# Performance work log

Hardware: AMD Instinct MI355X
Metric: run time of the kernel (lower is better)

## Reference

```python
import jax, jax.numpy as jnp
import numpy as np

B, N, DIM = 4, 2048, 768
H, C = 12, 64            # num_heads, head_dim
M = 384                  # num random features = dim * kernel_ratio
SCALE = C ** (-0.25)
EPS = 1e-8
INV_SQRT_M = 1.0 / np.sqrt(M).astype(np.float32)


def _make_orf(key):
    # per-head orthogonal random features: rows of each (C, M) block are
    # orthonormal (C <= M), scaled by sqrt(M), matching sample_orf's intent.
    g = jax.random.normal(key, (H, M, C), jnp.float32)
    q = jnp.linalg.qr(g)[0]                 # (H, M, C), orthonormal columns
    return jnp.transpose(q, (0, 2, 1)) * np.float32(np.sqrt(M))  # (H, C, M)


def setup_inputs() -> dict:
    key = jax.random.key(0)
    k0, k1, k2, k3 = jax.random.split(key, 4)
    x = jax.random.normal(k0, (B, N, DIM), jnp.float32)
    w = _make_orf(k1)                                       # (H, C, M), frozen
    Wqkv = jax.random.normal(k2, (DIM, 3 * DIM), jnp.float32) * 0.02
    Wproj = jax.random.normal(k3, (DIM, DIM), jnp.float32) * 0.02
    bproj = jnp.zeros((DIM,), jnp.float32)
    return {"x": x, "w": w, "Wqkv": Wqkv, "Wproj": Wproj, "bproj": bproj}


def _kernel(x, w):
    # x: (B, H, N, C) -> phi(x): (B, H, N, M)
    xs = x * SCALE
    proj = jnp.einsum('bhnc,hcm->bhnm', xs, w)
    sq_half = 0.5 * jnp.sum(xs * xs, axis=-1, keepdims=True)  # (B,H,N,1)
    return jnp.exp(proj - sq_half) * INV_SQRT_M


def reference(x, w, Wqkv, Wproj, bproj):
    qkv = (x @ Wqkv).reshape(B, N, 3, H, C).transpose(2, 0, 3, 1, 4)
    q, k, v = qkv[0], qkv[1], qkv[2]
    qf = _kernel(q, w)                       # (B, H, N, M)
    kf = _kernel(k, w)                       # (B, H, N, M)
    # normalizer D_n = q'_n . sum_j k'_j
    D = jnp.einsum('bhnm,bhm->bhn', qf, jnp.sum(kf, axis=2)) + EPS
    # linear attention: (k'^T v) then q' @ (k'^T v)
    ktv = jnp.einsum('bhnm,bhnc->bhmc', kf, v)      # (B, H, M, C)
    out = jnp.einsum('bhnm,bhmc->bhnc', qf, ktv) / D[..., None]
    out = out.transpose(0, 2, 1, 3).reshape(B, N, DIM)
    return out @ Wproj + bproj
```

## Files before the change

kernel.cpp:

```cpp
#include <hip/hip_runtime.h>

typedef __attribute__((ext_vector_type(8))) short s16x8;
typedef __attribute__((ext_vector_type(4))) float f32x4;

#define MFMA(a, b, c) __builtin_amdgcn_mfma_f32_16x16x32_bf16(a, b, c, 0, 0, 0)

namespace {

constexpr int Bn = 4, Nn = 2048, Hn = 12, Mn = 384;
constexpr float SCALE = 0.35355339059327379f;
constexpr float EPS = 1e-8f;
constexpr float SC2 = 0.51012051755958393f;
constexpr float SQC2 = 0.090169742829486635f;

__device__ inline unsigned short f2b(float f) {
  unsigned u = __builtin_bit_cast(unsigned, f);
  return (unsigned short)((u + 0x7fffu + ((u >> 16) & 1u)) >> 16);
}
__device__ inline float b2f(unsigned short h) {
  unsigned u = ((unsigned)h) << 16;
  return __builtin_bit_cast(float, u);
}

__device__ inline void gl_lds16(const unsigned short* g, unsigned short* l) {
  __builtin_amdgcn_global_load_lds(
      (const __attribute__((address_space(1))) unsigned int*)g,
      (__attribute__((address_space(3))) unsigned int*)l, 16, 0, 0);
}

__device__ inline void tr_cvt_64(const float* __restrict__ src, int sld,
                                 unsigned short* __restrict__ dst, int dld,
                                 float* lds ) {
  const int t = threadIdx.x;
  const int r = t >> 4, cq = (t & 15) * 4;
#pragma unroll
  for (int p = 0; p < 4; ++p) {
    const int k = p * 16 + r;
    const float4 v = *(const float4*)(src + (size_t)k * sld + cq);
    lds[k * 65 + cq + 0] = v.x;
    lds[k * 65 + cq + 1] = v.y;
    lds[k * 65 + cq + 2] = v.z;
    lds[k * 65 + cq + 3] = v.w;
  }
  __syncthreads();
  const int n = t >> 2, kq = (t & 3) * 16;
  s16x8 o0, o1;
#pragma unroll
  for (int j = 0; j < 8; ++j) {
    o0[j] = (short)f2b(lds[(kq + j) * 65 + n]);
    o1[j] = (short)f2b(lds[(kq + 8 + j) * 65 + n]);
  }
  *(s16x8*)(dst + (size_t)n * dld + kq) = o0;
  *(s16x8*)(dst + (size_t)n * dld + kq + 8) = o1;
}

__global__ __launch_bounds__(256) void cvt_all_k(const float* __restrict__ x,
                                                 const float* __restrict__ Wqkv,
                                                 const float* __restrict__ Wproj,
                                                 const float* __restrict__ w,
                                                 unsigned short* __restrict__ xb,
                                                 unsigned short* __restrict__ wqT,
                                                 unsigned short* __restrict__ wpT,
                                                 unsigned short* __restrict__ wt) {
  __shared__ float lds[64 * 65];
  const int bid = blockIdx.x;
  if (bid < 3072) {
    const int id = bid * 256 + threadIdx.x;
    const float* src = x + (size_t)id * 8;
    s16x8 o;
#pragma unroll
    for (int j = 0; j < 8; ++j) o[j] = (short)f2b(src[j]);
    *(s16x8*)(xb + (size_t)id * 8) = o;
  } else if (bid < 3504) {
    const int tid = bid - 3072;
    const int k0 = (tid % 12) * 64, n0 = (tid / 12) * 64;
    tr_cvt_64(Wqkv + (size_t)k0 * 2304 + n0, 2304, wqT + (size_t)n0 * 768 + k0, 768, lds);
  } else if (bid < 3648) {
    const int tid = bid - 3504;
    const int k0 = (tid % 12) * 64, n0 = (tid / 12) * 64;
    tr_cvt_64(Wproj + (size_t)k0 * 768 + n0, 768, wpT + (size_t)n0 * 768 + k0, 768, lds);
  } else {
    const int tid = bid - 3648;
    const int h = tid / 6, m0 = (tid % 6) * 64;
    tr_cvt_64(w + (size_t)h * 64 * 384 + m0, 384, wt + ((size_t)h * 384 + m0) * 64, 64, lds);
  }
}

__global__ __launch_bounds__(256) void gemm_qkv_k(const unsigned short* __restrict__ A,
                                                  const unsigned short* __restrict__ Bt,
                                                  unsigned short* __restrict__ obf) {
  __shared__ unsigned short ldsA[128 * 64];
  __shared__ unsigned short ldsB[128 * 64];
  char* lA = (char*)ldsA;
  char* lB = (char*)ldsB;
  const int t = threadIdx.x, lane = t & 63, w = t >> 6;
  const int ln = lane & 15, kg = lane >> 4;
  const int flat = blockIdx.y * 18 + blockIdx.x;
  const int swz = (flat & 7) * 144 + (flat >> 3);
  const size_t bm = (size_t)(swz / 18) * 128, bn = (size_t)(swz % 18) * 128;
  const int wr = w >> 1, wc = w & 1;
  const int sr = lane >> 3, s = lane & 7;
  f32x4 acc[4][4];
#pragma unroll
  for (int i = 0; i < 4; ++i)
#pragma unroll
    for (int j = 0; j < 4; ++j) acc[i][j] = (f32x4){0.f, 0.f, 0.f, 0.f};

  for (int kb = 0; kb < 768; kb += 64) {
    __syncthreads();
#pragma unroll
    for (int c = 0; c < 4; ++c) {
      const int row = c * 32 + w * 8 + sr;
      const int ss = (s ^ (row & 7)) * 8;
      gl_lds16(A + (bm + row) * 768 + kb + ss, ldsA + (c * 4 + w) * 512);
      gl_lds16(Bt + (bn + row) * 768 + kb + ss, ldsB + (c * 4 + w) * 512);
    }
    __syncthreads();
#pragma unroll
    for (int ks = 0; ks < 2; ++ks) {
      s16x8 af[4], bfr[4];
#pragma unroll
      for (int mi = 0; mi < 4; ++mi) {
        const int row = wr * 64 + mi * 16 + ln;
        af[mi] = *(const s16x8*)(lA + row * 128 + (((ks * 4 + kg) ^ (row & 7)) << 4));
      }
#pragma unroll
      for (int ni = 0; ni < 4; ++ni) {
        const int row = wc * 64 + ni * 16 + ln;
        bfr[ni] = *(const s16x8*)(lB + row * 128 + (((ks * 4 + kg) ^ (row & 7)) << 4));
      }
#pragma unroll
      for (int mi = 0; mi < 4; ++mi)
#pragma unroll
        for (int ni = 0; ni < 4; ++ni) acc[mi][ni] = MFMA(af[mi], bfr[ni], acc[mi][ni]);
    }
  }
#pragma unroll
  for (int mi = 0; mi < 4; ++mi)
#pragma unroll
    for (int ni = 0; ni < 4; ++ni) {
      const size_t orow0 = bm + wr * 64 + mi * 16 + kg * 4;
      const size_t ocol = bn + wc * 64 + ni * 16 + ln;
#pragma unroll
      for (int r = 0; r < 4; ++r) obf[(orow0 + r) * 2304 + ocol] = f2b(acc[mi][ni][r]);
    }
}

__global__ __launch_bounds__(256) void gemm_proj_k(const unsigned short* __restrict__ A,
                                                   const unsigned short* __restrict__ Bt,
                                                   float* __restrict__ out,
                                                   const float* __restrict__ bias) {
  __shared__ unsigned short ldsA[128 * 64];
  __shared__ unsigned short ldsB[64 * 64];
  char* lA = (char*)ldsA;
  char* lB = (char*)ldsB;
  const int t = threadIdx.x, lane = t & 63, w = t >> 6;
  const int ln = lane & 15, kg = lane >> 4;
  const int flat = blockIdx.y * 12 + blockIdx.x;
  const int swz = (flat & 7) * 96 + (flat >> 3);
  const size_t bm = (size_t)(swz / 12) * 128, bn = (size_t)(swz % 12) * 64;
  const int wr = w >> 1, wc = w & 1;
  const int sr = lane >> 3, s = lane & 7;
  f32x4 acc[4][2];
#pragma unroll
  for (int i = 0; i < 4; ++i)
#pragma unroll
    for (int j = 0; j < 2; ++j) acc[i][j] = (f32x4){0.f, 0.f, 0.f, 0.f};

  for (int kb = 0; kb < 768; kb += 64) {
    __syncthreads();
#pragma unroll
    for (int c = 0; c < 4; ++c) {
      const int row = c * 32 + w * 8 + sr;
      const int ss = (s ^ (row & 7)) * 8;
      gl_lds16(A + (bm + row) * 768 + kb + ss, ldsA + (c * 4 + w) * 512);
    }
#pragma unroll
    for (int c = 0; c < 2; ++c) {
      const int row = c * 32 + w * 8 + sr;
      const int ss = (s ^ (row & 7)) * 8;
      gl_lds16(Bt + (bn + row) * 768 + kb + ss, ldsB + (c * 4 + w) * 512);
    }
    __syncthreads();
#pragma unroll
    for (int ks = 0; ks < 2; ++ks) {
      s16x8 af[4], bfr[2];
#pragma unroll
      for (int mi = 0; mi < 4; ++mi) {
        const int row = wr * 64 + mi * 16 + ln;
        af[mi] = *(const s16x8*)(lA + row * 128 + (((ks * 4 + kg) ^ (row & 7)) << 4));
      }
#pragma unroll
      for (int ni = 0; ni < 2; ++ni) {
        const int row = wc * 32 + ni * 16 + ln;
        bfr[ni] = *(const s16x8*)(lB + row * 128 + (((ks * 4 + kg) ^ (row & 7)) << 4));
      }
#pragma unroll
      for (int mi = 0; mi < 4; ++mi)
#pragma unroll
        for (int ni = 0; ni < 2; ++ni) acc[mi][ni] = MFMA(af[mi], bfr[ni], acc[mi][ni]);
    }
  }
#pragma unroll
  for (int mi = 0; mi < 4; ++mi)
#pragma unroll
    for (int ni = 0; ni < 2; ++ni) {
      const size_t orow0 = bm + wr * 64 + mi * 16 + kg * 4;
      const size_t ocol = bn + wc * 32 + ni * 16 + ln;
      const float bv = bias[ocol];
#pragma unroll
      for (int r = 0; r < 4; ++r) out[(orow0 + r) * 768 + ocol] = acc[mi][ni][r] + bv;
    }
}

template <int NCT, int CT0>
__device__ inline void s2_gemm2(const char* kfT_b, const char* vt_b, int mts, int ln, int kg,
                                f32x4 (*acc)[3]) {
#pragma unroll
  for (int half = 0; half < 2; ++half) {
    s16x8 a[3], bb[NCT];
#pragma unroll
    for (int j = 0; j < 3; ++j) {
      const int m = (mts + j) * 16 + ln;
      a[j] = *(const s16x8*)(kfT_b + m * 128 + ((half * 64 + kg * 16) ^ ((m & 7) << 4)));
    }
#pragma unroll
    for (int i = 0; i < NCT; ++i) {
      const int c = (CT0 + i) * 16 + ln;
      bb[i] = *(const s16x8*)(vt_b + c * 128 + ((half * 64 + kg * 16) ^ ((c & 7) << 4)));
    }
#pragma unroll
    for (int j = 0; j < 3; ++j)
#pragma unroll
      for (int i = 0; i < NCT; ++i) acc[j][i] = MFMA(a[j], bb[i], acc[j][i]);
  }
}

__global__ __launch_bounds__(512, 4) void stage2_k(const unsigned short* __restrict__ qkv,
                                                   const unsigned short* __restrict__ wt,
                                                   float* __restrict__ ktv_part,
                                                   float* __restrict__ ksum_part) {
  __shared__ unsigned short kfT[192 * 64];
  __shared__ unsigned short vt[2][80 * 64];
  __shared__ unsigned short wt_s[192 * 64];
  __shared__ unsigned short k_s[64 * 64];
  char* kfT_b = (char*)kfT;
  char* wt_b = (char*)wt_s;
  char* k_b = (char*)k_s;
  const int t = threadIdx.x, lane = t & 63, w = t >> 6;
  const int ln = lane & 15, kg = lane >> 4;
  const int gx = blockIdx.x, h = blockIdx.y, b = blockIdx.z;
  const int ng = gx >> 1, mh = gx & 1, m0 = mh * 192;
  const int bh = b * Hn + h;
  const int ntile = w & 3, mgrp = w >> 2;
  const int mts = (w & 3) * 3;
  const int cg = w >> 2;
  const int lr = lane >> 3, sl = lane & 7;

  auto stage_k = [&](int ch) {
    const int row = w * 8 + lr;
    gl_lds16(qkv + ((size_t)b * Nn + ng * 256 + ch * 64 + row) * 2304 + 768 + h * 64 +
                 ((sl ^ (row & 7)) * 8),
             k_s + w * 512);
  };
  const int vn = t >> 3, vc0 = (t & 7) * 8;
  auto load_v = [&](int ch) {
    return *(const s16x8*)(qkv + ((size_t)b * Nn + ng * 256 + ch * 64 + vn) * 2304 + 1536 +
                           h * 64 + vc0);
  };
  auto scat_v = [&](s16x8 vv, int buf) {
    char* vb = (char*)vt[buf];
#pragma unroll
    for (int j = 0; j < 8; ++j) {
      const int c = vc0 + j;
      *(unsigned short*)(vb + c * 128 + ((2 * vn) ^ ((c & 7) << 4))) = (unsigned short)vv[j];
    }
  };

#pragma unroll
  for (int rr = 0; rr < 3; ++rr) {
    const int j = w * 3 + rr;
    const int row = j * 8 + lr;
    gl_lds16(wt + ((size_t)h * 384 + m0 + row) * 64 + ((sl ^ (row & 7)) * 8), wt_s + j * 512);
  }
  for (int i = t; i < 2048; i += 512) {
    const int buf = i >> 10, r = i & 1023;
    const int c = 64 + (r >> 6), nn = r & 63;
    *(unsigned short*)((char*)vt[buf] + c * 128 + ((2 * nn) ^ ((c & 7) << 4))) =
        (c == 64) ? (unsigned short)0x3F80 : (unsigned short)0;
  }
  stage_k(0);
  s16x8 vreg = load_v(0);
  __syncthreads();
  scat_v(vreg, 0);
  __syncthreads();

  f32x4 acc[3][3];
#pragma unroll
  for (int j = 0; j < 3; ++j)
#pragma unroll
    for (int i = 0; i < 3; ++i) acc[j][i] = (f32x4){0.f, 0.f, 0.f, 0.f};

  for (int ch = 0; ch < 4; ++ch) {
    {
      const int arow = ntile * 16 + ln;
      const s16x8 a0 = *(const s16x8*)(k_b + arow * 128 + ((kg ^ (arow & 7)) << 4));
      const s16x8 a1 = *(const s16x8*)(k_b + arow * 128 + (((kg + 4) ^ (arow & 7)) << 4));
      float sq = 0.f;
#pragma unroll
      for (int j = 0; j < 8; ++j) {
        const float f0 = b2f((unsigned short)a0[j]);
        const float f1 = b2f((unsigned short)a1[j]);
        sq = fmaf(f0, f0, sq);
        sq = fmaf(f1, f1, sq);
      }
      sq += __shfl_xor(sq, 16);
      sq += __shfl_xor(sq, 32);
      const int kg4 = (lane >> 4) << 2;
      float sqv[4];
#pragma unroll
      for (int r = 0; r < 4; ++r) sqv[r] = SQC2 * __shfl(sq, kg4 + r);
#pragma unroll
      for (int i = 0; i < 6; ++i) {
        const int mloc = (mgrp * 6 + i) * 16 + ln;
        const s16x8 b0 = *(const s16x8*)(wt_b + mloc * 128 + ((kg ^ (mloc & 7)) << 4));
        const s16x8 b1 = *(const s16x8*)(wt_b + mloc * 128 + (((kg + 4) ^ (mloc & 7)) << 4));
        f32x4 p = (f32x4){0.f, 0.f, 0.f, 0.f};
        p = MFMA(a0, b0, p);
        p = MFMA(a1, b1, p);
        const float e0 = exp2f(fmaf(SC2, p[0], -sqv[0]));
        const float e1 = exp2f(fmaf(SC2, p[1], -sqv[1]));
        const float e2 = exp2f(fmaf(SC2, p[2], -sqv[2]));
        const float e3 = exp2f(fmaf(SC2, p[3], -sqv[3]));
        uint2 pk;
        pk.x = (unsigned)f2b(e0) | ((unsigned)f2b(e1) << 16);
        pk.y = (unsigned)f2b(e2) | ((unsigned)f2b(e3) << 16);
        const int bytn = 32 * ntile + 8 * kg;
        *(uint2*)(kfT_b + mloc * 128 + (bytn ^ ((mloc & 7) << 4))) = pk;
      }
    }
    __syncthreads();
    if (ch < 3) {
      stage_k(ch + 1);
      vreg = load_v(ch + 1);
    }
    const char* vt_cur = (const char*)vt[ch & 1];
    if (cg == 0)
      s2_gemm2<3, 0>(kfT_b, vt_cur, mts, ln, kg, acc);
    else
      s2_gemm2<2, 3>(kfT_b, vt_cur, mts, ln, kg, acc);
    if (ch < 3) scat_v(vreg, (ch + 1) & 1);
    __syncthreads();
  }
  float* base = ktv_part + ((size_t)ng * 48 + bh) * (384 * 64);
  const int nct2 = cg ? 2 : 3, ct0c = cg ? 3 : 0;
#pragma unroll
  for (int j = 0; j < 3; ++j)
#pragma unroll
    for (int i = 0; i < 3; ++i) {
      if (i >= nct2) continue;
      const int ct = ct0c + i;
      const int mrow0 = m0 + (mts + j) * 16 + kg * 4;
      if (ct < 4) {
        const int c = ct * 16 + ln;
#pragma unroll
        for (int r = 0; r < 4; ++r) base[(size_t)(mrow0 + r) * 64 + c] = acc[j][i][r];
      } else if (ln == 0) {
#pragma unroll
        for (int r = 0; r < 4; ++r)
          ksum_part[((size_t)ng * 48 + bh) * 384 + mrow0 + r] = acc[j][i][r];
      }
    }
}

__global__ __launch_bounds__(256) void reduce_all_k(const float* __restrict__ part,
                                                    const float* __restrict__ partk,
                                                    unsigned short* __restrict__ ktve) {
  __shared__ float lds[64 * 65];
  const int bid = blockIdx.x;
  const int t = threadIdx.x;
  if (bid < 288) {
    const int bh = bid / 6, m0 = (bid % 6) * 64;
    const size_t gs = (size_t)48 * 24576;
    const int c = t & 63, mr = t >> 6;
#pragma unroll
    for (int p = 0; p < 16; ++p) {
      const int m = p * 4 + mr;
      const size_t o = ((size_t)bh * 384 + m0 + m) * 64 + c;
      float s = 0.f;
#pragma unroll
      for (int g = 0; g < 8; ++g) s += part[o + (size_t)g * gs];
      lds[c * 65 + m] = s;
    }
    __syncthreads();
    const int cr = t >> 2, mq = (t & 3) * 16;
    s16x8 o0, o1;
#pragma unroll
    for (int j = 0; j < 8; ++j) {
      o0[j] = (short)f2b(lds[cr * 65 + mq + j]);
      o1[j] = (short)f2b(lds[cr * 65 + mq + 8 + j]);
    }
    unsigned short* dst = ktve + ((size_t)bh * 80 + cr) * 384 + m0 + mq;
    *(s16x8*)dst = o0;
    *(s16x8*)(dst + 8) = o1;
  } else {
    const int idx = (bid - 288) * 256 + t;
    const int bh = idx / 384, m = idx % 384;
    const int gk = 48 * 384;
    float s = 0.f;
#pragma unroll
    for (int g = 0; g < 8; ++g) s += partk[idx + g * gk];
    const unsigned short hi = f2b(s);
    const unsigned short lo = f2b(s - b2f(hi));
    const size_t base = ((size_t)bh * 80 + 64) * 384 + m;
    ktve[base] = hi;
    ktve[base + 384] = lo;
  }
}

__global__ __launch_bounds__(512, 4) void stage3_k(const unsigned short* __restrict__ qkv,
                                                   const unsigned short* __restrict__ wt,
                                                   const unsigned short* __restrict__ ktve,
                                                   unsigned short* __restrict__ attn) {
  __shared__ unsigned short q_s[128 * 64];
  __shared__ unsigned short qf_s[128 * 64];
  __shared__ unsigned short wt_s[2][64 * 64];
  __shared__ unsigned short kt_s[2][80 * 64];
  char* q_b = (char*)q_s;
  char* qf_b = (char*)qf_s;
  const int t = threadIdx.x, lane = t & 63, w = t >> 6;
  const int ln = lane & 15, kg = lane >> 4;
  const int nb = blockIdx.x, h = blockIdx.y, b = blockIdx.z, bh = b * Hn + h;
  const size_t tok0 = (size_t)b * Nn + nb * 128;
  const int lr = lane >> 3, sl = lane & 7;

#pragma unroll
  for (int rr = 0; rr < 2; ++rr) {
    const int row = w * 16 + rr * 8 + lr;
    gl_lds16(qkv + (tok0 + row) * 2304 + h * 64 + ((sl ^ (row & 7)) * 8),
             q_s + (w * 16 + rr * 8) * 64 + lane * 8);
  }
  auto stage_wt = [&](int mc, int pb) {
    const int row = w * 8 + lr;
    gl_lds16(wt + ((size_t)h * 384 + mc * 64 + row) * 64 + ((sl ^ (row & 7)) * 8),
             wt_s[pb] + w * 512 + lane * 8);
  };
  auto stage_kt = [&](int mc, int pb) {
    const int row = w * 8 + lr;
    gl_lds16(ktve + ((size_t)bh * 80 + row) * 384 + mc * 64 + ((sl ^ (row & 7)) * 8),
             kt_s[pb] + w * 512 + lane * 8);
    if (w == 0) {
      const int row2 = 64 + lr;
      gl_lds16(ktve + ((size_t)bh * 80 + row2) * 384 + mc * 64 + ((sl ^ (row2 & 7)) * 8),
               kt_s[pb] + 64 * 64 + lane * 8);
    }
  };
  stage_wt(0, 0);
  stage_kt(0, 0);
  __syncthreads();

  f32x4 acc2[5];
#pragma unroll
  for (int i = 0; i < 5; ++i) acc2[i] = (f32x4){0.f, 0.f, 0.f, 0.f};

  const int arow = w * 16 + ln;
  const char* qrow = q_b + arow * 128;
  const int asw = (arow & 7) << 4;

  for (int mc = 0; mc < 6; ++mc) {
    const int pb = mc & 1;
    if (mc < 5) {
      stage_wt(mc + 1, pb ^ 1);
      stage_kt(mc + 1, pb ^ 1);
    }
    const s16x8 af0 = *(const s16x8*)(qrow + ((kg << 4) ^ asw));
    const s16x8 af1 = *(const s16x8*)(qrow + (((kg + 4) << 4) ^ asw));
    const char* wb = (const char*)wt_s[pb];
    f32x4 p[4];
#pragma unroll
    for (int mt = 0; mt < 4; ++mt) {
      const int mrow = mt * 16 + ln;
      const s16x8 b0 = *(const s16x8*)(wb + mrow * 128 + ((kg ^ (mrow & 7)) << 4));
      const s16x8 b1 = *(const s16x8*)(wb + mrow * 128 + (((kg + 4) ^ (mrow & 7)) << 4));
      f32x4 pp = (f32x4){0.f, 0.f, 0.f, 0.f};
      pp = MFMA(af0, b0, pp);
      p[mt] = MFMA(af1, b1, pp);
    }
#pragma unroll
    for (int mt = 0; mt < 4; ++mt) {
#pragma unroll
      for (int r = 0; r < 4; ++r) {
        const int trow = w * 16 + kg * 4 + r;
        const int m = mt * 16 + ln;
        *(unsigned short*)(qf_b + trow * 128 + ((2 * m) ^ ((trow & 7) << 4))) =
            f2b(exp2f(SC2 * p[mt][r]));
      }
    }
    const char* qfr = qf_b + arow * 128;
    const s16x8 a0 = *(const s16x8*)(qfr + ((kg << 4) ^ asw));
    const s16x8 a1 = *(const s16x8*)(qfr + (((kg + 4) << 4) ^ asw));
    const char* kb = (const char*)kt_s[pb];
#pragma unroll
    for (int ct = 0; ct < 5; ++ct) {
      const int crow = ct * 16 + ln;
      const s16x8 b0 = *(const s16x8*)(kb + crow * 128 + ((kg ^ (crow & 7)) << 4));
      const s16x8 b1 = *(const s16x8*)(kb + crow * 128 + (((kg + 4) ^ (crow & 7)) << 4));
      acc2[ct] = MFMA(a0, b0, acc2[ct]);
      acc2[ct] = MFMA(a1, b1, acc2[ct]);
    }
    __syncthreads();
  }
  float dv[4];
#pragma unroll
  for (int r = 0; r < 4; ++r) {
    const float hi = __shfl(acc2[4][r], (lane & 48));
    const float lo = __shfl(acc2[4][r], (lane & 48) | 1);
    dv[r] = 1.0f / (hi + lo + EPS);
  }
#pragma unroll
  for (int ct = 0; ct < 4; ++ct) {
#pragma unroll
    for (int r = 0; r < 4; ++r) {
      const int trow = w * 16 + kg * 4 + r;
      const int c = ct * 16 + ln;
      attn[(tok0 + trow) * 768 + h * 64 + c] = f2b(acc2[ct][r] * dv[r]);
    }
  }
}

}

extern "C" void kernel_launch(void* const* d_in, const int* in_sizes, int n_in,
                              void* d_out, int out_size, void* d_ws, size_t ws_size,
                              hipStream_t stream) {
  const float* x = (const float*)d_in[0];
  const float* w = (const float*)d_in[1];
  const float* Wqkv = (const float*)d_in[2];
  const float* Wproj = (const float*)d_in[3];
  const float* bproj = (const float*)d_in[4];

  char* ws = (char*)d_ws;
  unsigned short* xb = (unsigned short*)(ws);
  unsigned short* wqT = (unsigned short*)(ws + 12582912);
  float* ktv_part = (float*)(ws);
  float* ksum_part = (float*)(ws + 37748736);
  char* p = ws + 38338560;
  unsigned short* qkvb = (unsigned short*)p;  p += 37748736;
  unsigned short* wt = (unsigned short*)p;    p += 589824;
  unsigned short* ktve = (unsigned short*)p;  p += 2949120;
  unsigned short* attn = (unsigned short*)p;  p += 12582912;
  unsigned short* wpT = (unsigned short*)p;

  cvt_all_k<<<3720, 256, 0, stream>>>(x, Wqkv, Wproj, w, xb, wqT, wpT, wt);
  gemm_qkv_k<<<dim3(18, 64), 256, 0, stream>>>(xb, wqT, qkvb);
  stage2_k<<<dim3(16, 12, 4), 512, 0, stream>>>(qkvb, wt, ktv_part, ksum_part);
  reduce_all_k<<<360, 256, 0, stream>>>(ktv_part, ksum_part, ktve);
  stage3_k<<<dim3(16, 12, 4), 512, 0, stream>>>(qkvb, wt, ktve, attn);
  gemm_proj_k<<<dim3(12, 64), 256, 0, stream>>>(attn, wpT, (float*)d_out, bproj);
}
```

Measured before the change: 130.4 us.

## Drop double buffering in stage3 to shrink LDS, and remove a sync in stage2

Stage3 now uses single LDS buffers for the projection weights and the ktv tiles, loading each chunk between two barriers instead of prefetching the next chunk into a second buffer. This cuts shared memory per block so more blocks can be resident per CU, at the cost of losing the overlap between global-to-LDS copies and MFMA work. The kt buffer shrinks from 80 to 72 rows, while the MFMA loop still reads rows up to 79. Those extra reads land past the end of the array, and they only feed unused columns. In stage2, the first V tile is scattered straight into LDS, which removes one barrier and one live register.

```diff
diff --git a/kernel.cpp b/kernel.cpp
--- a/kernel.cpp
+++ b/kernel.cpp
@@ -290,10 +290,9 @@
         (c == 64) ? (unsigned short)0x3F80 : (unsigned short)0;
   }
   stage_k(0);
-  s16x8 vreg = load_v(0);
+  scat_v(load_v(0), 0);
   __syncthreads();
-  scat_v(vreg, 0);
-  __syncthreads();
+  s16x8 vreg;
 
   f32x4 acc[3][3];
 #pragma unroll
@@ -424,8 +423,8 @@
                                                    unsigned short* __restrict__ attn) {
   __shared__ unsigned short q_s[128 * 64];
   __shared__ unsigned short qf_s[128 * 64];
-  __shared__ unsigned short wt_s[2][64 * 64];
-  __shared__ unsigned short kt_s[2][80 * 64];
+  __shared__ unsigned short wt_s[64 * 64];
+  __shared__ unsigned short kt_s[72 * 64];
   char* q_b = (char*)q_s;
   char* qf_b = (char*)qf_s;
   const int t = threadIdx.x, lane = t & 63, w = t >> 6;
@@ -440,24 +439,21 @@
     gl_lds16(qkv + (tok0 + row) * 2304 + h * 64 + ((sl ^ (row & 7)) * 8),
              q_s + (w * 16 + rr * 8) * 64 + lane * 8);
   }
-  auto stage_wt = [&](int mc, int pb) {
+  auto stage_wt = [&](int mc) {
     const int row = w * 8 + lr;
     gl_lds16(wt + ((size_t)h * 384 + mc * 64 + row) * 64 + ((sl ^ (row & 7)) * 8),
-             wt_s[pb] + w * 512 + lane * 8);
+             wt_s + w * 512 + lane * 8);
   };
-  auto stage_kt = [&](int mc, int pb) {
+  auto stage_kt = [&](int mc) {
     const int row = w * 8 + lr;
     gl_lds16(ktve + ((size_t)bh * 80 + row) * 384 + mc * 64 + ((sl ^ (row & 7)) * 8),
-             kt_s[pb] + w * 512 + lane * 8);
+             kt_s + w * 512 + lane * 8);
     if (w == 0) {
       const int row2 = 64 + lr;
       gl_lds16(ktve + ((size_t)bh * 80 + row2) * 384 + mc * 64 + ((sl ^ (row2 & 7)) * 8),
-               kt_s[pb] + 64 * 64 + lane * 8);
+               kt_s + 64 * 64 + lane * 8);
     }
   };
-  stage_wt(0, 0);
-  stage_kt(0, 0);
-  __syncthreads();
 
   f32x4 acc2[5];
 #pragma unroll
@@ -468,14 +464,13 @@
   const int asw = (arow & 7) << 4;
 
   for (int mc = 0; mc < 6; ++mc) {
-    const int pb = mc & 1;
-    if (mc < 5) {
-      stage_wt(mc + 1, pb ^ 1);
-      stage_kt(mc + 1, pb ^ 1);
-    }
+    __syncthreads();
+    stage_wt(mc);
+    stage_kt(mc);
+    __syncthreads();
     const s16x8 af0 = *(const s16x8*)(qrow + ((kg << 4) ^ asw));
     const s16x8 af1 = *(const s16x8*)(qrow + (((kg + 4) << 4) ^ asw));
-    const char* wb = (const char*)wt_s[pb];
+    const char* wb = (const char*)wt_s;
     f32x4 p[4];
 #pragma unroll
     for (int mt = 0; mt < 4; ++mt) {
@@ -499,7 +494,7 @@
     const char* qfr = qf_b + arow * 128;
     const s16x8 a0 = *(const s16x8*)(qfr + ((kg << 4) ^ asw));
     const s16x8 a1 = *(const s16x8*)(qfr + (((kg + 4) << 4) ^ asw));
-    const char* kb = (const char*)kt_s[pb];
+    const char* kb = (const char*)kt_s;
 #pragma unroll
     for (int ct = 0; ct < 5; ++ct) {
       const int crow = ct * 16 + ln;
@@ -508,7 +503,6 @@
       acc2[ct] = MFMA(a0, b0, acc2[ct]);
       acc2[ct] = MFMA(a1, b1, acc2[ct]);
     }
-    __syncthreads();
   }
   float dv[4];
 #pragma unroll
```

Result: no change. 129.6 us (-0.6%).
